# Kernel optimization log

Hardware: AMD Instinct MI355X
Metric: run time of the kernel (lower is better)

## Reference

```python
import jax, jax.numpy as jnp
import numpy as np

V, N, D, K = 4, 2048, 128, 10
NEG = -1e9


def setup_inputs() -> dict:
    key = jax.random.key(0)
    k1, k2, k3, k4, k5 = jax.random.split(key, 5)
    aligned = jax.random.normal(k1, (V, N, D), dtype=jnp.float32)
    C = jax.random.uniform(k2, (V, V, N, N), dtype=jnp.float32)
    s = 1.0 / np.sqrt(D)
    WQ = jax.random.normal(k3, (V, D, D), dtype=jnp.float32) * s
    WK = jax.random.normal(k4, (V, D, D), dtype=jnp.float32) * s
    WV = jax.random.normal(k5, (V, D, D), dtype=jnp.float32) * s
    return {"aligned": aligned, "C": C, "WQ": WQ, "WK": WK, "WV": WV}


def _forward(aligned, C, WQ, WK, WV):
    # per-view linear projections (nn.Linear: x @ W^T), W: (V, out, in)
    Qn = jnp.einsum('vnd,ved->vne', aligned, WQ)  # (V,N,D)
    Kn = jnp.einsum('vnd,ved->vne', aligned, WK)
    Vn = jnp.einsum('vnd,ved->vne', aligned, WV)

    # per-pair row-wise top-k sparsify + row-normalize
    vals, idx = jax.lax.top_k(C, K)  # (V,V,N,K)
    pi = jnp.arange(V)[:, None, None, None]
    qi = jnp.arange(V)[None, :, None, None]
    ri = jnp.arange(N)[None, None, :, None]
    sparse = jnp.zeros_like(C).at[pi, qi, ri, idx].set(vals)
    row_sum = sparse.sum(axis=3, keepdims=True) + 1e-12
    C_hat = sparse / row_sum
    # diagonal (p == q) blocks stay all-zero in the original loop
    offdiag = (1.0 - jnp.eye(V, dtype=C.dtype))[:, :, None, None]
    C_hat = C_hat * offdiag

    # full pairwise scores (p queries attend to q keys)
    scores = jnp.einsum('pnd,qmd->pqnm', Qn, Kn) / jnp.sqrt(jnp.float32(D))
    mask = (C_hat > 0).astype(scores.dtype)
    scores = scores * mask + (1.0 - mask) * NEG
    alpha = jax.nn.softmax(scores, axis=3)  # (V,V,N,N)

    # aggregate: sum over source views q (diagonal gives uniform avg of Vn[p])
    nbr = jnp.einsum('pqnm,qmd->pnd', alpha, Vn)  # (V,N,D)
    return nbr


def reference(aligned, C, WQ, WK, WV):
    return _forward(aligned, C, WQ, WK, WV)
```

## Files before the change

kernel.cpp:

```cpp
#include <hip/hip_runtime.h>
#include <cstdint>
#include <cstddef>

#define VV 4
#define NN 2048
#define DDIM 128
#define KK 10
#define CAP 256

__device__ __forceinline__ bool kgt(float v1, int i1, float v0, int i0) {
  return (v1 > v0) || (v1 == v0 && i1 < i0);
}

__global__ __launch_bounds__(256) void proj_kernel(
    const float* __restrict__ A, const float* __restrict__ WQ,
    const float* __restrict__ WK, const float* __restrict__ WV,
    float* __restrict__ Qn, float* __restrict__ Kn, float* __restrict__ Vn,
    float* __restrict__ partialMV)
{
  __shared__ float As[16][DDIM];
  __shared__ float Ws[3][16][129];
  __shared__ float s_mv[2][DDIM];

  const int t    = threadIdx.x;
  const int v    = blockIdx.x >> 7;
  const int blk  = blockIdx.x & 127;
  const int n0   = blk * 16;
  const int e    = t & 127;
  const int half = t >> 7;

  float accq[8], acck[8], accv[8];
#pragma unroll
  for (int r = 0; r < 8; ++r) { accq[r] = 0.f; acck[r] = 0.f; accv[r] = 0.f; }

  const float* Ab = A + ((size_t)v * NN + n0) * DDIM;
#pragma unroll
  for (int k = 0; k < 2; ++k) {
    int id4 = k * 256 + t;
    int r   = id4 >> 5;
    int d4  = id4 & 31;
    float4 a4 = *(const float4*)(Ab + (size_t)id4 * 4);
    *(float4*)&As[r][d4 * 4] = a4;
  }
  const float* wqb = WQ + (size_t)v * DDIM * DDIM;
  const float* wkb = WK + (size_t)v * DDIM * DDIM;
  const float* wvb = WV + (size_t)v * DDIM * DDIM;

  for (int d0 = 0; d0 < DDIM; d0 += 16) {
    __syncthreads();
#pragma unroll
    for (int k = 0; k < 2; ++k) {
      int id4 = k * 256 + t;
      int ee  = id4 >> 2;
      int c4  = id4 & 3;
      const float4 wq4 = *(const float4*)(wqb + (size_t)ee * DDIM + d0 + c4 * 4);
      const float4 wk4 = *(const float4*)(wkb + (size_t)ee * DDIM + d0 + c4 * 4);
      const float4 wv4 = *(const float4*)(wvb + (size_t)ee * DDIM + d0 + c4 * 4);
      int dd = c4 * 4;
      Ws[0][dd + 0][ee] = wq4.x; Ws[0][dd + 1][ee] = wq4.y;
      Ws[0][dd + 2][ee] = wq4.z; Ws[0][dd + 3][ee] = wq4.w;
      Ws[1][dd + 0][ee] = wk4.x; Ws[1][dd + 1][ee] = wk4.y;
      Ws[1][dd + 2][ee] = wk4.z; Ws[1][dd + 3][ee] = wk4.w;
      Ws[2][dd + 0][ee] = wv4.x; Ws[2][dd + 1][ee] = wv4.y;
      Ws[2][dd + 2][ee] = wv4.z; Ws[2][dd + 3][ee] = wv4.w;
    }
    __syncthreads();
#pragma unroll
    for (int dd = 0; dd < 16; dd += 4) {
      float4 a[8];
#pragma unroll
      for (int r = 0; r < 8; ++r) a[r] = *(const float4*)&As[half * 8 + r][d0 + dd];
#pragma unroll
      for (int c = 0; c < 4; ++c) {
        float wq = Ws[0][dd + c][e];
        float wk = Ws[1][dd + c][e];
        float wv = Ws[2][dd + c][e];
#pragma unroll
        for (int r = 0; r < 8; ++r) {
          float av = ((const float*)&a[r])[c];
          accq[r] = fmaf(av, wq, accq[r]);
          acck[r] = fmaf(av, wk, acck[r]);
          accv[r] = fmaf(av, wv, accv[r]);
        }
      }
    }
  }

  const size_t ob = ((size_t)v * NN + n0 + half * 8) * DDIM + e;
#pragma unroll
  for (int r = 0; r < 8; ++r) {
    Qn[ob + (size_t)r * DDIM] = accq[r];
    Kn[ob + (size_t)r * DDIM] = acck[r];
    Vn[ob + (size_t)r * DDIM] = accv[r];
  }
  float s = 0.f;
#pragma unroll
  for (int r = 0; r < 8; ++r) s += accv[r];
  s_mv[half][e] = s;
  __syncthreads();
  if (half == 0)
    partialMV[((size_t)v * 128 + blk) * DDIM + e] = s + s_mv[1][e];
}

__global__ __launch_bounds__(256) void fused_kernel(
    const float* __restrict__ C, const float* __restrict__ Qn,
    const float* __restrict__ Kn, const float* __restrict__ Vn,
    const float* __restrict__ partialMV, float* __restrict__ out)
{
  __shared__ float    s_val[4][CAP];
  __shared__ int      s_idx[4][CAP];
  __shared__ unsigned s_cnt[4];
  __shared__ float    s_sc[4][32];
  __shared__ float    s_al[4][32];
  __shared__ int      s_sel[4][32];
  __shared__ float    s_mvp[2][DDIM];
  __shared__ float    s_mv[DDIM];

  const int t    = threadIdx.x;
  const int w    = t >> 6;
  const int lane = t & 63;
  const int task = blockIdx.x * 4 + w;
  const int p    = task >> 11;
  const int n    = task & 2047;
  const float SCALE = 0.08838834764831845f;

  {
    const int e    = t & 127;
    const int half = t >> 7;
    const float* pb = partialMV + (size_t)p * 128 * DDIM;
    float sum = 0.f;
    for (int b = half * 64; b < half * 64 + 64; ++b)
      sum += pb[(size_t)b * DDIM + e];
    s_mvp[half][e] = sum;
    __syncthreads();
    if (half == 0) s_mv[e] = (s_mvp[0][e] + s_mvp[1][e]) * (1.0f / 2048.0f);
    __syncthreads();
  }

  for (int o = 0; o < 3; ++o) {
    const int q = o + (o >= p ? 1 : 0);
    const float* row = C + (((size_t)(p * 4 + q) * NN + n) << 11);
    float4 vv[8];
#pragma unroll
    for (int i = 0; i < 8; ++i) vv[i] = *(const float4*)(row + i * 256 + lane * 4);
    if (lane == 0) s_cnt[w] = 0u;

    const float T1 = 0.99f, T2 = 0.95f;
    int c1 = 0;
#pragma unroll
    for (int i = 0; i < 8; ++i) {
      const float* pv = (const float*)&vv[i];
#pragma unroll
      for (int c = 0; c < 4; ++c) c1 += (pv[c] > T1) ? 1 : 0;
    }
#pragma unroll
    for (int off = 32; off; off >>= 1) c1 += __shfl_xor(c1, off);

    float T = T1; int cnt = c1; bool ok = (c1 >= KK && c1 <= CAP);
    if (!ok) {
      int c2 = 0;
#pragma unroll
      for (int i = 0; i < 8; ++i) {
        const float* pv = (const float*)&vv[i];
#pragma unroll
        for (int c = 0; c < 4; ++c) c2 += (pv[c] > T2) ? 1 : 0;
      }
#pragma unroll
      for (int off = 32; off; off >>= 1) c2 += __shfl_xor(c2, off);
      T = T2; cnt = c2; ok = (c2 >= KK && c2 <= CAP);
    }

    if (ok) {
#pragma unroll
      for (int i = 0; i < 8; ++i) {
        const float* pv = (const float*)&vv[i];
#pragma unroll
        for (int c = 0; c < 4; ++c) {
          float x = pv[c];
          if (x > T) {
            unsigned pos = atomicAdd(&s_cnt[w], 1u);
            s_val[w][pos] = x;
            s_idx[w][pos] = i * 256 + lane * 4 + c;
          }
        }
      }
      __threadfence_block();
      if (cnt <= 64) {
        float kv = (lane < cnt) ? s_val[w][lane] : -1e30f;
        int   ki = (lane < cnt) ? s_idx[w][lane] : 0x7FFFFFFF;
#pragma unroll
        for (int k = 2; k <= 64; k <<= 1) {
#pragma unroll
          for (int j = k >> 1; j > 0; j >>= 1) {
            float ov = __shfl_xor(kv, j);
            int   oi = __shfl_xor(ki, j);
            bool dirDesc = (lane & k) == 0;
            bool lower   = (lane & j) == 0;
            bool ogt     = (ov > kv) || (ov == kv && oi < ki);
            bool take    = (dirDesc == lower) ? ogt : !ogt;
            if (take) { kv = ov; ki = oi; }
          }
        }
        if (lane < KK) s_sel[w][o * KK + lane] = ki;
      } else {
        float rv[4]; int ri[4];
#pragma unroll
        for (int s = 0; s < 4; ++s) {
          int  sl = lane + s * 64;
          bool in = sl < cnt;
          rv[s] = in ? s_val[w][sl] : -1e30f;
          ri[s] = in ? s_idx[w][sl] : 0x7FFFFFFF;
        }
        for (int r = 0; r < KK; ++r) {
          float lv = rv[0]; int li = ri[0]; int ls = 0;
#pragma unroll
          for (int s = 1; s < 4; ++s)
            if (kgt(rv[s], ri[s], lv, li)) { lv = rv[s]; li = ri[s]; ls = s; }
          float mv = lv; int mi = li;
#pragma unroll
          for (int off = 1; off < 64; off <<= 1) {
            float ov = __shfl_xor(mv, off);
            int   oi = __shfl_xor(mi, off);
            if (kgt(ov, oi, mv, mi)) { mv = ov; mi = oi; }
          }
          if (lane == 0) s_sel[w][o * KK + r] = mi;
          if (li == mi) {
#pragma unroll
            for (int s = 0; s < 4; ++s)
              if (ls == s) { rv[s] = -1e30f; ri[s] = 0x7FFFFFFF; }
          }
        }
      }
    } else {
      unsigned consumed = 0;
      for (int r = 0; r < KK; ++r) {
        float lv = -1e30f; int li = 0x7FFFFFFF; int ls = 0;
#pragma unroll
        for (int i = 0; i < 8; ++i) {
          const float* pv = (const float*)&vv[i];
#pragma unroll
          for (int c = 0; c < 4; ++c) {
            int   sl = i * 4 + c;
            float x  = ((consumed >> sl) & 1u) ? -1e30f : pv[c];
            int   ix = i * 256 + lane * 4 + c;
            if (kgt(x, ix, lv, li)) { lv = x; li = ix; ls = sl; }
          }
        }
        float mv = lv; int mi = li;
#pragma unroll
        for (int off = 1; off < 64; off <<= 1) {
          float ov = __shfl_xor(mv, off);
          int   oi = __shfl_xor(mi, off);
          if (kgt(ov, oi, mv, mi)) { mv = ov; mi = oi; }
        }
        if (lane == 0) s_sel[w][o * KK + r] = mi;
        if (li == mi) consumed |= (1u << ls);
      }
    }
    __threadfence_block();
  }

  const float* qrow = Qn + ((size_t)p * NN + n) * DDIM;
  const float q0 = qrow[lane];
  const float q1 = qrow[lane + 64];

#pragma unroll
  for (int o = 0; o < 3; ++o) {
    const int q = o + (o >= p ? 1 : 0);
    const float* Kb = Kn + (size_t)q * NN * DDIM;
#pragma unroll
    for (int j = 0; j < KK; ++j) {
      const float* kr = Kb + (size_t)s_sel[w][o * KK + j] * DDIM;
      float s = q0 * kr[lane] + q1 * kr[lane + 64];
#pragma unroll
      for (int off = 32; off; off >>= 1) s += __shfl_xor(s, off);
      if (lane == 0) s_sc[w][o * KK + j] = s * SCALE;
    }
  }
  __threadfence_block();

  if (lane < 30) {
    const int b = (lane / KK) * KK;
    float m = s_sc[w][b];
#pragma unroll
    for (int j = 1; j < KK; ++j) m = fmaxf(m, s_sc[w][b + j]);
    float den = 0.f;
#pragma unroll
    for (int j = 0; j < KK; ++j) den += expf(s_sc[w][b + j] - m);
    s_al[w][lane] = expf(s_sc[w][lane] - m) / den;
  }
  __threadfence_block();

  float acc0 = s_mv[lane];
  float acc1 = s_mv[lane + 64];
#pragma unroll
  for (int o = 0; o < 3; ++o) {
    const int q = o + (o >= p ? 1 : 0);
    const float* Vb = Vn + (size_t)q * NN * DDIM;
#pragma unroll
    for (int j = 0; j < KK; ++j) {
      const float a = s_al[w][o * KK + j];
      const float* vr = Vb + (size_t)s_sel[w][o * KK + j] * DDIM;
      acc0 = fmaf(a, vr[lane], acc0);
      acc1 = fmaf(a, vr[lane + 64], acc1);
    }
  }
  float* orow = out + ((size_t)p * NN + n) * DDIM;
  orow[lane]      = acc0;
  orow[lane + 64] = acc1;
}

extern "C" void kernel_launch(void* const* d_in, const int* in_sizes, int n_in,
                              void* d_out, int out_size, void* d_ws, size_t ws_size,
                              hipStream_t stream)
{
  const float* A  = (const float*)d_in[0];
  const float* C  = (const float*)d_in[1];
  const float* WQ = (const float*)d_in[2];
  const float* WK = (const float*)d_in[3];
  const float* WV = (const float*)d_in[4];
  float* out = (float*)d_out;

  char* ws = (char*)d_ws;
  float* Qn        = (float*)ws;
  float* Kn        = (float*)(ws + (size_t)4 * 1024 * 1024);
  float* Vn        = (float*)(ws + (size_t)8 * 1024 * 1024);
  float* partialMV = (float*)(ws + (size_t)12 * 1024 * 1024);

  hipLaunchKernelGGL(proj_kernel, dim3(512), dim3(256), 0, stream,
                     A, WQ, WK, WV, Qn, Kn, Vn, partialMV);
  hipLaunchKernelGGL(fused_kernel, dim3(2048), dim3(256), 0, stream,
                     C, Qn, Kn, Vn, partialMV, out);
}
```

Measured before the change: 413.5 us.

## Precompute mean-V in a separate kernel and vectorize gather loads in fused kernel

```diff
diff --git a/kernel.cpp b/kernel.cpp
--- a/kernel.cpp
+++ b/kernel.cpp
@@ -7,6 +7,8 @@
 #define DDIM 128
 #define KK 10
 #define CAP 256
+
+#define WAVE_LDS_SYNC() asm volatile("s_waitcnt lgkmcnt(0)" ::: "memory")
 
 __device__ __forceinline__ bool kgt(float v1, int i1, float v0, int i0) {
   return (v1 > v0) || (v1 == v0 && i1 < i0);
@@ -102,10 +104,27 @@
     partialMV[((size_t)v * 128 + blk) * DDIM + e] = s + s_mv[1][e];
 }
 
+__global__ __launch_bounds__(128) void meanv_kernel(
+    const float* __restrict__ partialMV, float* __restrict__ meanV)
+{
+  const int v = blockIdx.x;
+  const int e = threadIdx.x;
+  const float* pb = partialMV + (size_t)v * 128 * DDIM + e;
+  float s0 = 0.f, s1 = 0.f, s2 = 0.f, s3 = 0.f;
+#pragma unroll 8
+  for (int b = 0; b < 128; b += 4) {
+    s0 += pb[(size_t)(b + 0) * DDIM];
+    s1 += pb[(size_t)(b + 1) * DDIM];
+    s2 += pb[(size_t)(b + 2) * DDIM];
+    s3 += pb[(size_t)(b + 3) * DDIM];
+  }
+  meanV[v * DDIM + e] = (s0 + s1 + s2 + s3) * (1.0f / 2048.0f);
+}
+
 __global__ __launch_bounds__(256) void fused_kernel(
     const float* __restrict__ C, const float* __restrict__ Qn,
     const float* __restrict__ Kn, const float* __restrict__ Vn,
-    const float* __restrict__ partialMV, float* __restrict__ out)
+    const float* __restrict__ meanV, float* __restrict__ out)
 {
   __shared__ float    s_val[4][CAP];
   __shared__ int      s_idx[4][CAP];
@@ -113,8 +132,7 @@
   __shared__ float    s_sc[4][32];
   __shared__ float    s_al[4][32];
   __shared__ int      s_sel[4][32];
-  __shared__ float    s_mvp[2][DDIM];
-  __shared__ float    s_mv[DDIM];
+  __shared__ __align__(16) float s_mv[DDIM];
 
   const int t    = threadIdx.x;
   const int w    = t >> 6;
@@ -124,18 +142,8 @@
   const int n    = task & 2047;
   const float SCALE = 0.08838834764831845f;
 
-  {
-    const int e    = t & 127;
-    const int half = t >> 7;
-    const float* pb = partialMV + (size_t)p * 128 * DDIM;
-    float sum = 0.f;
-    for (int b = half * 64; b < half * 64 + 64; ++b)
-      sum += pb[(size_t)b * DDIM + e];
-    s_mvp[half][e] = sum;
-    __syncthreads();
-    if (half == 0) s_mv[e] = (s_mvp[0][e] + s_mvp[1][e]) * (1.0f / 2048.0f);
-    __syncthreads();
-  }
+  if (t < DDIM) s_mv[t] = meanV[p * DDIM + t];
+  __syncthreads();
 
   for (int o = 0; o < 3; ++o) {
     const int q = o + (o >= p ? 1 : 0);
@@ -184,7 +192,7 @@
           }
         }
       }
-      __threadfence_block();
+      WAVE_LDS_SYNC();
       if (cnt <= 64) {
         float kv = (lane < cnt) ? s_val[w][lane] : -1e30f;
         int   ki = (lane < cnt) ? s_idx[w][lane] : 0x7FFFFFFF;
@@ -257,27 +265,33 @@
         if (li == mi) consumed |= (1u << ls);
       }
     }
-    __threadfence_block();
+    WAVE_LDS_SYNC();
   }
 
   const float* qrow = Qn + ((size_t)p * NN + n) * DDIM;
-  const float q0 = qrow[lane];
-  const float q1 = qrow[lane + 64];
+  float2 q2 = *(const float2*)(qrow + 2 * lane);
+  q2.x *= SCALE; q2.y *= SCALE;
 
 #pragma unroll
   for (int o = 0; o < 3; ++o) {
     const int q = o + (o >= p ? 1 : 0);
     const float* Kb = Kn + (size_t)q * NN * DDIM;
+    int    sel[KK];
+    float2 kv2[KK];
 #pragma unroll
     for (int j = 0; j < KK; ++j) {
-      const float* kr = Kb + (size_t)s_sel[w][o * KK + j] * DDIM;
-      float s = q0 * kr[lane] + q1 * kr[lane + 64];
+      sel[j] = s_sel[w][o * KK + j];
+      kv2[j] = *(const float2*)(Kb + (size_t)sel[j] * DDIM + 2 * lane);
+    }
+#pragma unroll
+    for (int j = 0; j < KK; ++j) {
+      float s = q2.x * kv2[j].x + q2.y * kv2[j].y;
 #pragma unroll
       for (int off = 32; off; off >>= 1) s += __shfl_xor(s, off);
-      if (lane == 0) s_sc[w][o * KK + j] = s * SCALE;
-    }
-  }
-  __threadfence_block();
+      if (lane == 0) s_sc[w][o * KK + j] = s;
+    }
+  }
+  WAVE_LDS_SYNC();
 
   if (lane < 30) {
     const int b = (lane / KK) * KK;
@@ -286,28 +300,31 @@
     for (int j = 1; j < KK; ++j) m = fmaxf(m, s_sc[w][b + j]);
     float den = 0.f;
 #pragma unroll
-    for (int j = 0; j < KK; ++j) den += expf(s_sc[w][b + j] - m);
-    s_al[w][lane] = expf(s_sc[w][lane] - m) / den;
-  }
-  __threadfence_block();
-
-  float acc0 = s_mv[lane];
-  float acc1 = s_mv[lane + 64];
+    for (int j = 0; j < KK; ++j) den += __expf(s_sc[w][b + j] - m);
+    s_al[w][lane] = __expf(s_sc[w][lane] - m) / den;
+  }
+  WAVE_LDS_SYNC();
+
+  float2 acc = *(const float2*)&s_mv[2 * lane];
 #pragma unroll
   for (int o = 0; o < 3; ++o) {
     const int q = o + (o >= p ? 1 : 0);
     const float* Vb = Vn + (size_t)q * NN * DDIM;
+    float2 vv2[KK]; float al[KK];
 #pragma unroll
     for (int j = 0; j < KK; ++j) {
-      const float a = s_al[w][o * KK + j];
-      const float* vr = Vb + (size_t)s_sel[w][o * KK + j] * DDIM;
-      acc0 = fmaf(a, vr[lane], acc0);
-      acc1 = fmaf(a, vr[lane + 64], acc1);
+      int s  = s_sel[w][o * KK + j];
+      al[j]  = s_al[w][o * KK + j];
+      vv2[j] = *(const float2*)(Vb + (size_t)s * DDIM + 2 * lane);
+    }
+#pragma unroll
+    for (int j = 0; j < KK; ++j) {
+      acc.x = fmaf(al[j], vv2[j].x, acc.x);
+      acc.y = fmaf(al[j], vv2[j].y, acc.y);
     }
   }
   float* orow = out + ((size_t)p * NN + n) * DDIM;
-  orow[lane]      = acc0;
-  orow[lane + 64] = acc1;
+  *(float2*)(orow + 2 * lane) = acc;
 }
 
 extern "C" void kernel_launch(void* const* d_in, const int* in_sizes, int n_in,
@@ -326,9 +343,12 @@
   float* Kn        = (float*)(ws + (size_t)4 * 1024 * 1024);
   float* Vn        = (float*)(ws + (size_t)8 * 1024 * 1024);
   float* partialMV = (float*)(ws + (size_t)12 * 1024 * 1024);
+  float* meanV     = (float*)(ws + (size_t)12 * 1024 * 1024 + 256 * 1024);
 
   hipLaunchKernelGGL(proj_kernel, dim3(512), dim3(256), 0, stream,
                      A, WQ, WK, WV, Qn, Kn, Vn, partialMV);
+  hipLaunchKernelGGL(meanv_kernel, dim3(4), dim3(128), 0, stream,
+                     partialMV, meanV);
   hipLaunchKernelGGL(fused_kernel, dim3(2048), dim3(256), 0, stream,
-                     C, Qn, Kn, Vn, partialMV, out);
-}
+                     C, Qn, Kn, Vn, meanV, out);
+}
```

After: 396.2 us. 4.2% less time.
